# Kernel optimization log

Measured on AMD Instinct MI355X. Metric: run time of the kernel, lower is better.

Reference implementation:

```python
import jax, jax.numpy as jnp
import numpy as np

B, D, H, G = 32768, 768, 256, 8
GS = D // G          # group size = 96
MIN_G, MAX_G = 2, 6  # min/max active groups


def setup_inputs() -> dict:
    key = jax.random.key(0)
    ks = jax.random.split(key, 12)
    s = 0.02
    return {
        "query_embedding": jax.random.normal(ks[0], (B, D), jnp.float32),
        # router_net: Linear(D,H) -> LayerNorm(H) -> GELU -> Linear(H,H//2) -> GELU -> Linear(H//2,G)
        "w1": jax.random.normal(ks[1], (D, H), jnp.float32) * s,
        "b1": jnp.zeros((H,), jnp.float32),
        "ln_g": jnp.ones((H,), jnp.float32),
        "ln_b": jnp.zeros((H,), jnp.float32),
        "w2": jax.random.normal(ks[2], (H, H // 2), jnp.float32) * s,
        "b2": jnp.zeros((H // 2,), jnp.float32),
        "w3": jax.random.normal(ks[3], (H // 2, G), jnp.float32) * s,
        "b3": jnp.zeros((G,), jnp.float32),
        # dim_importance: Linear(D,H) -> GELU -> Linear(H,D) (bias init 2.0) -> Sigmoid
        "dw1": jax.random.normal(ks[4], (D, H), jnp.float32) * s,
        "db1": jnp.zeros((H,), jnp.float32),
        "dw2": jax.random.normal(ks[5], (H, D), jnp.float32) * s,
        "db2": jnp.full((D,), 2.0, jnp.float32),
        "group_importance": jax.random.normal(ks[6], (G,), jnp.float32) * s,
    }


def _gelu(x):
    return jax.nn.gelu(x, approximate=False)  # torch nn.GELU default = exact erf


def _layernorm(x, g, b, eps=1e-5):
    mu = jnp.mean(x, axis=-1, keepdims=True)
    var = jnp.var(x, axis=-1, keepdims=True)
    return (x - mu) * jax.lax.rsqrt(var + eps) * g + b


def reference(query_embedding, w1, b1, ln_g, ln_b, w2, b2, w3, b3,
              dw1, db1, dw2, db2, group_importance):
    x = query_embedding
    # router_net (eval mode: dropout is identity, sigmoid gating not gumbel)
    h1 = _gelu(_layernorm(x @ w1 + b1, ln_g, ln_b))
    h2 = _gelu(h1 @ w2 + b2)
    group_logits = h2 @ w3 + b3 + group_importance          # [B, G]
    group_probs = jax.nn.sigmoid(group_logits)

    # constrained hard selection: top MIN_G always on; ranks MIN_G..MAX_G-1 on iff prob > 0.5
    order = jnp.argsort(-group_probs, axis=-1)              # descending sort indices [B, G]
    sorted_probs = jnp.take_along_axis(group_probs, order, axis=-1)
    ranks = jnp.arange(G)
    act_sorted = jnp.where(ranks < MIN_G, 1.0,
                           jnp.where(ranks < MAX_G,
                                     (sorted_probs > 0.5).astype(jnp.float32), 0.0))
    b_idx = jnp.arange(x.shape[0])[:, None]
    hard_mask = jnp.zeros_like(group_probs).at[b_idx, order].set(act_sorted)
    # straight-through estimator
    group_selection = hard_mask - jax.lax.stop_gradient(group_probs) + group_probs

    # expand each group decision over its group_size dims -> [B, D]
    group_mask = jnp.repeat(group_selection, GS, axis=-1)

    dim_weights = jax.nn.sigmoid(_gelu(x @ dw1 + db1) @ dw2 + db2)  # [B, D]
    mask = group_mask * dim_weights

    active_groups = jnp.mean(jnp.sum((group_probs > 0.5).astype(jnp.float32), axis=-1))
    group_usage = jnp.mean((group_probs > 0.5).astype(jnp.float32), axis=0)
    f = jnp.mean(group_probs, axis=0)
    load_balance = G * jnp.sum(f * (1.0 / G))
    active_dims = jnp.mean(jnp.sum((mask > 0.5).astype(jnp.float32), axis=-1))

    return (mask, group_mask, dim_weights, group_probs, group_selection,
            active_groups, group_usage, load_balance, active_dims)
```

## Files before the change

### kernel.cpp

```cpp
#include <hip/hip_runtime.h>
#include <math.h>

#define NB 32768
#define ND 768
#define NH 256
#define NG 8
#define GSZ 96

typedef __attribute__((ext_vector_type(8))) short short8_t;
typedef __attribute__((ext_vector_type(4))) float f32x4;

__device__ __forceinline__ float gelu_exact(float v) {
    return 0.5f * v * (1.0f + erff(v * 0.7071067811865475f));
}
__device__ __forceinline__ float sigmoidf_(float v) {
    return 1.0f / (1.0f + expf(-v));
}
__device__ __forceinline__ unsigned short f2bf(float f) {
    union { float f; unsigned u; } a; a.f = f;
    unsigned r = a.u + 0x7FFF + ((a.u >> 16) & 1);
    return (unsigned short)(r >> 16);
}
__device__ __forceinline__ void f2bf2(float f, unsigned short& hi, unsigned short& lo) {
    union { float f; unsigned u; } a; a.f = f;
    unsigned r = a.u + 0x7FFF + ((a.u >> 16) & 1);
    hi = (unsigned short)(r >> 16);
    union { unsigned u; float f; } hf; hf.u = (r >> 16) << 16;
    float rem = f - hf.f;
    union { float f; unsigned u; } b; b.f = rem;
    unsigned r2 = b.u + 0x7FFF + ((b.u >> 16) & 1);
    lo = (unsigned short)(r2 >> 16);
}

__global__ __launch_bounds__(256) void cvt_wall(
    const float* __restrict__ w1, const float* __restrict__ dw1,
    const float* __restrict__ dw2, const float* __restrict__ w2,
    unsigned short* __restrict__ w1Th, unsigned short* __restrict__ w1Tl,
    unsigned short* __restrict__ dw1T, unsigned short* __restrict__ dw2T,
    unsigned short* __restrict__ w2Th, unsigned short* __restrict__ w2Tl,
    float* __restrict__ scal)
{
    const int b = blockIdx.x, t = threadIdx.x;
    if (b < 96) {
        int idx = b * 256 + t;
        int k8 = idx >> 8, c = idx & 255;
        short8_t h, lo;
        #pragma unroll
        for (int j = 0; j < 8; ++j) {
            unsigned short hi_, lo_;
            f2bf2(w1[(size_t)(k8 * 8 + j) * 256 + c], hi_, lo_);
            h[j] = (short)hi_; lo[j] = (short)lo_;
        }
        *(short8_t*)(w1Th + (size_t)c * 768 + k8 * 8) = h;
        *(short8_t*)(w1Tl + (size_t)c * 768 + k8 * 8) = lo;
    } else if (b < 192) {
        int idx = (b - 96) * 256 + t;
        int k8 = idx >> 8, c = idx & 255;
        short8_t h;
        #pragma unroll
        for (int j = 0; j < 8; ++j)
            h[j] = (short)f2bf(dw1[(size_t)(k8 * 8 + j) * 256 + c]);
        *(short8_t*)(dw1T + (size_t)c * 768 + k8 * 8) = h;
    } else if (b < 288) {
        int idx = (b - 192) * 256 + t;
        int k8 = idx / 768, c = idx - k8 * 768;
        short8_t h;
        #pragma unroll
        for (int j = 0; j < 8; ++j)
            h[j] = (short)f2bf(dw2[(size_t)(k8 * 8 + j) * 768 + c]);
        *(short8_t*)(dw2T + (size_t)c * 256 + k8 * 8) = h;
    } else if (b < 304) {
        int idx = (b - 288) * 256 + t;
        int k8 = idx >> 7, c = idx & 127;
        short8_t h, lo;
        #pragma unroll
        for (int j = 0; j < 8; ++j) {
            unsigned short hi_, lo_;
            f2bf2(w2[(size_t)(k8 * 8 + j) * 128 + c], hi_, lo_);
            h[j] = (short)hi_; lo[j] = (short)lo_;
        }
        *(short8_t*)(w2Th + (size_t)c * 256 + k8 * 8) = h;
        *(short8_t*)(w2Tl + (size_t)c * 256 + k8 * 8) = lo;
    } else {
        if (t < 11) scal[t] = 0.0f;
    }
}

__global__ __launch_bounds__(512) void mfma_pair(
    const float* __restrict__ x,
    const unsigned short* __restrict__ w1Th, const unsigned short* __restrict__ w1Tl,
    const unsigned short* __restrict__ dw1T, const float* __restrict__ db1,
    float* __restrict__ u1, unsigned short* __restrict__ g1h)
{
    __shared__ unsigned short Ah[128][40];
    __shared__ unsigned short Al[128][40];
    __shared__ unsigned short Bh[256][40];
    __shared__ unsigned short Bl[256][40];

    const int tid = threadIdx.x;
    const int l = tid & 63;
    const int w = tid >> 6;
    const int wm = w >> 2, wn = w & 3;
    const int lg = l >> 4, lr = l & 15;
    const bool splitRole = blockIdx.x < 256;
    const int rowsBase = (blockIdx.x & 255) * 128;

    f32x4 acc[4][4];
    #pragma unroll
    for (int mi = 0; mi < 4; ++mi)
        #pragma unroll
        for (int ni = 0; ni < 4; ++ni) acc[mi][ni] = (f32x4){0.f, 0.f, 0.f, 0.f};

    const int sArow = tid >> 2, sAseg = tid & 3;

    for (int kb = 0; kb < ND; kb += 32) {
        {
            const float* src = x + (size_t)(rowsBase + sArow) * ND + kb + sAseg * 8;
            float4 v0 = *(const float4*)src;
            float4 v1 = *(const float4*)(src + 4);
            float f[8] = {v0.x, v0.y, v0.z, v0.w, v1.x, v1.y, v1.z, v1.w};
            if (splitRole) {
                short8_t ph, pl;
                #pragma unroll
                for (int j = 0; j < 8; ++j) {
                    unsigned short hi_, lo_;
                    f2bf2(f[j], hi_, lo_);
                    ph[j] = (short)hi_; pl[j] = (short)lo_;
                }
                *(short8_t*)&Ah[sArow][sAseg * 8] = ph;
                *(short8_t*)&Al[sArow][sAseg * 8] = pl;
            } else {
                short8_t ph;
                #pragma unroll
                for (int j = 0; j < 8; ++j) ph[j] = (short)f2bf(f[j]);
                *(short8_t*)&Ah[sArow][sAseg * 8] = ph;
            }
        }
        #pragma unroll
        for (int m = 0; m < 2; ++m) {
            int flat = m * 512 + tid;
            int col = flat >> 2, seg = flat & 3;
            size_t off = (size_t)col * ND + kb + seg * 8;
            if (splitRole) {
                *(short8_t*)&Bh[col][seg * 8] = *(const short8_t*)(w1Th + off);
                *(short8_t*)&Bl[col][seg * 8] = *(const short8_t*)(w1Tl + off);
            } else {
                *(short8_t*)&Bh[col][seg * 8] = *(const short8_t*)(dw1T + off);
            }
        }
        __syncthreads();

        short8_t afh[4], bfh[4];
        #pragma unroll
        for (int mi = 0; mi < 4; ++mi)
            afh[mi] = *(const short8_t*)&Ah[wm * 64 + mi * 16 + lr][lg * 8];
        #pragma unroll
        for (int ni = 0; ni < 4; ++ni)
            bfh[ni] = *(const short8_t*)&Bh[wn * 64 + ni * 16 + lr][lg * 8];
        if (splitRole) {
            short8_t afl[4], bfl[4];
            #pragma unroll
            for (int mi = 0; mi < 4; ++mi)
                afl[mi] = *(const short8_t*)&Al[wm * 64 + mi * 16 + lr][lg * 8];
            #pragma unroll
            for (int ni = 0; ni < 4; ++ni)
                bfl[ni] = *(const short8_t*)&Bl[wn * 64 + ni * 16 + lr][lg * 8];
            #pragma unroll
            for (int mi = 0; mi < 4; ++mi)
                #pragma unroll
                for (int ni = 0; ni < 4; ++ni) {
                    acc[mi][ni] = __builtin_amdgcn_mfma_f32_16x16x32_bf16(
                        afl[mi], bfh[ni], acc[mi][ni], 0, 0, 0);
                    acc[mi][ni] = __builtin_amdgcn_mfma_f32_16x16x32_bf16(
                        afh[mi], bfl[ni], acc[mi][ni], 0, 0, 0);
                    acc[mi][ni] = __builtin_amdgcn_mfma_f32_16x16x32_bf16(
                        afh[mi], bfh[ni], acc[mi][ni], 0, 0, 0);
                }
        } else {
            #pragma unroll
            for (int mi = 0; mi < 4; ++mi)
                #pragma unroll
                for (int ni = 0; ni < 4; ++ni)
                    acc[mi][ni] = __builtin_amdgcn_mfma_f32_16x16x32_bf16(
                        afh[mi], bfh[ni], acc[mi][ni], 0, 0, 0);
        }
        __syncthreads();
    }

    if (splitRole) {
        #pragma unroll
        for (int ni = 0; ni < 4; ++ni) {
            int col = wn * 64 + ni * 16 + lr;
            #pragma unroll
            for (int mi = 0; mi < 4; ++mi) {
                int rbase = rowsBase + wm * 64 + mi * 16 + lg * 4;
                #pragma unroll
                for (int j = 0; j < 4; ++j)
                    u1[(size_t)(rbase + j) * 256 + col] = acc[mi][ni][j];
            }
        }
    } else {
        #pragma unroll
        for (int ni = 0; ni < 4; ++ni) {
            int col = wn * 64 + ni * 16 + lr;
            float bv = db1[col];
            #pragma unroll
            for (int mi = 0; mi < 4; ++mi) {
                int rbase = rowsBase + wm * 64 + mi * 16 + lg * 4;
                #pragma unroll
                for (int j = 0; j < 4; ++j)
                    g1h[(size_t)(rbase + j) * 256 + col] =
                        f2bf(gelu_exact(acc[mi][ni][j] + bv));
            }
        }
    }
}

__global__ __launch_bounds__(256) void k1_epi(
    const float* __restrict__ u1, const float* __restrict__ b1,
    const float* __restrict__ lng, const float* __restrict__ lnb,
    float* __restrict__ h1)
{
    const int wv = threadIdx.x >> 6, l = threadIdx.x & 63;
    const int row = blockIdx.x * 4 + wv;
    float4 a = *(const float4*)(u1 + (size_t)row * 256 + l * 4);
    float4 bb = *(const float4*)(b1 + l * 4);
    float u[4] = {a.x + bb.x, a.y + bb.y, a.z + bb.z, a.w + bb.w};
    float s = u[0] + u[1] + u[2] + u[3];
    float q = u[0]*u[0] + u[1]*u[1] + u[2]*u[2] + u[3]*u[3];
    #pragma unroll
    for (int o = 1; o < 64; o <<= 1) {
        s += __shfl_xor(s, o);
        q += __shfl_xor(q, o);
    }
    float mean = s * (1.0f / 256.0f);
    float var  = q * (1.0f / 256.0f) - mean * mean;
    float rstd = rsqrtf(var + 1e-5f);
    float4 g = *(const float4*)(lng + l * 4);
    float4 be = *(const float4*)(lnb + l * 4);
    float4 o;
    o.x = gelu_exact((u[0] - mean) * rstd * g.x + be.x);
    o.y = gelu_exact((u[1] - mean) * rstd * g.y + be.y);
    o.z = gelu_exact((u[2] - mean) * rstd * g.z + be.z);
    o.w = gelu_exact((u[3] - mean) * rstd * g.w + be.w);
    *(float4*)(h1 + (size_t)row * 256 + l * 4) = o;
}

__global__ __launch_bounds__(256) void mfma_u2(
    const float* __restrict__ h1, const unsigned short* __restrict__ BTh,
    const unsigned short* __restrict__ BTl, float* __restrict__ u2)
{
    __shared__ unsigned short Ah[128][40];
    __shared__ unsigned short Al[128][40];
    __shared__ unsigned short Bh[128][40];
    __shared__ unsigned short Bl[128][40];

    const int tid = threadIdx.x;
    const int l = tid & 63;
    const int w = tid >> 6;
    const int wm = w >> 1, wn = w & 1;
    const int lg = l >> 4, lr = l & 15;
    const int rowsBase = blockIdx.x * 128;

    f32x4 acc[4][4];
    #pragma unroll
    for (int mi = 0; mi < 4; ++mi)
        #pragma unroll
        for (int ni = 0; ni < 4; ++ni) acc[mi][ni] = (f32x4){0.f, 0.f, 0.f, 0.f};

    for (int kb = 0; kb < 256; kb += 32) {
        #pragma unroll
        for (int m = 0; m < 2; ++m) {
            int flat = m * 256 + tid;
            int row = flat >> 2, seg = flat & 3;
            const float* src = h1 + (size_t)(rowsBase + row) * 256 + kb + seg * 8;
            float4 v0 = *(const float4*)src;
            float4 v1 = *(const float4*)(src + 4);
            float f[8] = {v0.x, v0.y, v0.z, v0.w, v1.x, v1.y, v1.z, v1.w};
            short8_t ph, pl;
            #pragma unroll
            for (int j = 0; j < 8; ++j) {
                unsigned short hi_, lo_;
                f2bf2(f[j], hi_, lo_);
                ph[j] = (short)hi_; pl[j] = (short)lo_;
            }
            *(short8_t*)&Ah[row][seg * 8] = ph;
            *(short8_t*)&Al[row][seg * 8] = pl;
        }
        #pragma unroll
        for (int m = 0; m < 2; ++m) {
            int flat = m * 256 + tid;
            int col = flat >> 2, seg = flat & 3;
            size_t off = (size_t)col * 256 + kb + seg * 8;
            *(short8_t*)&Bh[col][seg * 8] = *(const short8_t*)(BTh + off);
            *(short8_t*)&Bl[col][seg * 8] = *(const short8_t*)(BTl + off);
        }
        __syncthreads();

        short8_t afh[4], afl[4], bfh[4], bfl[4];
        #pragma unroll
        for (int mi = 0; mi < 4; ++mi) {
            afh[mi] = *(const short8_t*)&Ah[wm * 64 + mi * 16 + lr][lg * 8];
            afl[mi] = *(const short8_t*)&Al[wm * 64 + mi * 16 + lr][lg * 8];
        }
        #pragma unroll
        for (int ni = 0; ni < 4; ++ni) {
            bfh[ni] = *(const short8_t*)&Bh[wn * 64 + ni * 16 + lr][lg * 8];
            bfl[ni] = *(const short8_t*)&Bl[wn * 64 + ni * 16 + lr][lg * 8];
        }
        #pragma unroll
        for (int mi = 0; mi < 4; ++mi)
            #pragma unroll
            for (int ni = 0; ni < 4; ++ni) {
                acc[mi][ni] = __builtin_amdgcn_mfma_f32_16x16x32_bf16(
                    afl[mi], bfh[ni], acc[mi][ni], 0, 0, 0);
                acc[mi][ni] = __builtin_amdgcn_mfma_f32_16x16x32_bf16(
                    afh[mi], bfl[ni], acc[mi][ni], 0, 0, 0);
                acc[mi][ni] = __builtin_amdgcn_mfma_f32_16x16x32_bf16(
                    afh[mi], bfh[ni], acc[mi][ni], 0, 0, 0);
            }
        __syncthreads();
    }

    #pragma unroll
    for (int ni = 0; ni < 4; ++ni) {
        int col = wn * 64 + ni * 16 + lr;
        #pragma unroll
        for (int mi = 0; mi < 4; ++mi) {
            int rbase = rowsBase + wm * 64 + mi * 16 + lg * 4;
            #pragma unroll
            for (int j = 0; j < 4; ++j)
                u2[(size_t)(rbase + j) * 128 + col] = acc[mi][ni][j];
        }
    }
}

__global__ __launch_bounds__(128) void k3_router(
    const float* __restrict__ u2, const float* __restrict__ w3,
    const float* __restrict__ b3, const float* __restrict__ gi,
    const float* __restrict__ b2, float* __restrict__ probsOut,
    float* __restrict__ selOut, float* __restrict__ scal)
{
    __shared__ float ws3[128][8];
    __shared__ float sAct[2], sP[2], sCnt[2][8];

    const int tid = threadIdx.x;
    *(float4*)&ws3[tid][0] = *(const float4*)(w3 + tid * 8);
    *(float4*)&ws3[tid][4] = *(const float4*)(w3 + tid * 8 + 4);
    __syncthreads();

    const int row = blockIdx.x * 128 + tid;
    const float* r0p = u2 + (size_t)row * 128;

    float accg[8];
    #pragma unroll
    for (int g = 0; g < 8; ++g) accg[g] = 0.0f;
    #pragma unroll 4
    for (int k4 = 0; k4 < 32; ++k4) {
        float4 a = *(const float4*)(r0p + k4 * 4);
        float4 bb = *(const float4*)(b2 + k4 * 4);
        float hv4[4];
        hv4[0] = gelu_exact(a.x + bb.x);
        hv4[1] = gelu_exact(a.y + bb.y);
        hv4[2] = gelu_exact(a.z + bb.z);
        hv4[3] = gelu_exact(a.w + bb.w);
        #pragma unroll
        for (int t = 0; t < 4; ++t)
            #pragma unroll
            for (int g = 0; g < 8; ++g)
                accg[g] = fmaf(hv4[t], ws3[k4 * 4 + t][g], accg[g]);
    }

    float p[8], gs[8], cnt[8];
    float actCnt = 0.0f, pSum = 0.0f;
    #pragma unroll
    for (int g = 0; g < 8; ++g) {
        float lg = accg[g] + b3[g] + gi[g];
        p[g] = sigmoidf_(lg);
    }
    #pragma unroll
    for (int g = 0; g < 8; ++g) {
        int rank = 0;
        #pragma unroll
        for (int j = 0; j < 8; ++j) {
            rank += (p[j] > p[g]) ? 1 : 0;
            rank += (j < g && p[j] == p[g]) ? 1 : 0;
        }
        float act = (rank < 2) ? 1.0f
                  : ((rank < 6) ? ((p[g] > 0.5f) ? 1.0f : 0.0f) : 0.0f);
        gs[g] = (act - p[g]) + p[g];
        float over = (p[g] > 0.5f) ? 1.0f : 0.0f;
        cnt[g] = over;
        actCnt += over;
        pSum += p[g];
    }

    *(float4*)(probsOut + (size_t)row * 8)     = *(float4*)&p[0];
    *(float4*)(probsOut + (size_t)row * 8 + 4) = *(float4*)&p[4];
    *(float4*)(selOut   + (size_t)row * 8)     = *(float4*)&gs[0];
    *(float4*)(selOut   + (size_t)row * 8 + 4) = *(float4*)&gs[4];

    #pragma unroll
    for (int o = 32; o > 0; o >>= 1) {
        actCnt += __shfl_down(actCnt, o);
        pSum   += __shfl_down(pSum, o);
        #pragma unroll
        for (int g = 0; g < 8; ++g) cnt[g] += __shfl_down(cnt[g], o);
    }
    if ((tid & 63) == 0) {
        int w = tid >> 6;
        sAct[w] = actCnt; sP[w] = pSum;
        #pragma unroll
        for (int g = 0; g < 8; ++g) sCnt[w][g] = cnt[g];
    }
    __syncthreads();
    if (tid == 0) {
        const float invB = 1.0f / 32768.0f;
        atomicAdd(&scal[0], (sAct[0] + sAct[1]) * invB);
        atomicAdd(&scal[9], (sP[0] + sP[1]) * invB);
        #pragma unroll
        for (int g = 0; g < 8; ++g)
            atomicAdd(&scal[1 + g], (sCnt[0][g] + sCnt[1][g]) * invB);
    }
}

__global__ __launch_bounds__(512) void mfma_dw2m(
    const unsigned short* __restrict__ g1h, const unsigned short* __restrict__ dw2T,
    const float* __restrict__ db2, const float* __restrict__ sel,
    float* __restrict__ dwts, float* __restrict__ maskOut,
    float* __restrict__ activeDims)
{
    __shared__ unsigned short As[128][40];
    __shared__ unsigned short Bs[256][40];
    __shared__ float sc[8];

    const int tid = threadIdx.x;
    const int l = tid & 63;
    const int w = tid >> 6;
    const int wm = w >> 2, wn = w & 3;
    const int lg = l >> 4, lr = l & 15;
    const int rb = blockIdx.x / 3, cb = blockIdx.x - rb * 3;
    const int rowsBase = rb * 128, colBase = cb * 256;

    f32x4 acc[4][4];
    #pragma unroll
    for (int mi = 0; mi < 4; ++mi)
        #pragma unroll
        for (int ni = 0; ni < 4; ++ni) acc[mi][ni] = (f32x4){0.f, 0.f, 0.f, 0.f};

    const int sArow = tid >> 2, sAseg = tid & 3;

    for (int kb = 0; kb < 256; kb += 32) {
        *(short8_t*)&As[sArow][sAseg * 8] =
            *(const short8_t*)(g1h + (size_t)(rowsBase + sArow) * 256 + kb + sAseg * 8);
        #pragma unroll
        for (int m = 0; m < 2; ++m) {
            int flat = m * 512 + tid;
            int col = flat >> 2, seg = flat & 3;
            *(short8_t*)&Bs[col][seg * 8] =
                *(const short8_t*)(dw2T + (size_t)(colBase + col) * 256 + kb + seg * 8);
        }
        __syncthreads();

        short8_t af[4], bf[4];
        #pragma unroll
        for (int mi = 0; mi < 4; ++mi)
            af[mi] = *(const short8_t*)&As[wm * 64 + mi * 16 + lr][lg * 8];
        #pragma unroll
        for (int ni = 0; ni < 4; ++ni)
            bf[ni] = *(const short8_t*)&Bs[wn * 64 + ni * 16 + lr][lg * 8];
        #pragma unroll
        for (int mi = 0; mi < 4; ++mi)
            #pragma unroll
            for (int ni = 0; ni < 4; ++ni)
                acc[mi][ni] = __builtin_amdgcn_mfma_f32_16x16x32_bf16(
                    af[mi], bf[ni], acc[mi][ni], 0, 0, 0);
        __syncthreads();
    }

    float cntF = 0.0f;
    #pragma unroll
    for (int ni = 0; ni < 4; ++ni) {
        int col = colBase + wn * 64 + ni * 16 + lr;
        float bv = db2[col];
        int g = col / GSZ;
        #pragma unroll
        for (int mi = 0; mi < 4; ++mi) {
            int rbase = rowsBase + wm * 64 + mi * 16 + lg * 4;
            #pragma unroll
            for (int j = 0; j < 4; ++j) {
                int row = rbase + j;
                float v = sigmoidf_(acc[mi][ni][j] + bv);
                dwts[(size_t)row * 768 + col] = v;
                float m = sel[(size_t)row * 8 + g] * v;
                maskOut[(size_t)row * 768 + col] = m;
                cntF += (m > 0.5f) ? 1.0f : 0.0f;
            }
        }
    }
    #pragma unroll
    for (int o = 32; o > 0; o >>= 1) cntF += __shfl_down(cntF, o);
    if ((tid & 63) == 0) sc[tid >> 6] = cntF;
    __syncthreads();
    if (tid == 0)
        atomicAdd(activeDims, (sc[0] + sc[1] + sc[2] + sc[3] +
                               sc[4] + sc[5] + sc[6] + sc[7]) * (1.0f / 32768.0f));
}

__global__ __launch_bounds__(256) void k4_gmask(
    const float* __restrict__ sel, float* __restrict__ gmaskOut)
{
    const int stride = gridDim.x * 256;
    for (int i4 = blockIdx.x * 256 + threadIdx.x; i4 < 6291456; i4 += stride) {
        int row = i4 / 192;
        int rem = i4 - row * 192;
        int g = rem / 24;
        float v = sel[(size_t)row * 8 + g];
        float4 gm = {v, v, v, v};
        *(float4*)(gmaskOut + (size_t)i4 * 4) = gm;
    }
}

extern "C" void kernel_launch(void* const* d_in, const int* in_sizes, int n_in,
                              void* d_out, int out_size, void* d_ws, size_t ws_size,
                              hipStream_t stream)
{
    const float* x   = (const float*)d_in[0];
    const float* w1  = (const float*)d_in[1];
    const float* b1  = (const float*)d_in[2];
    const float* lng = (const float*)d_in[3];
    const float* lnb = (const float*)d_in[4];
    const float* w2  = (const float*)d_in[5];
    const float* b2  = (const float*)d_in[6];
    const float* w3  = (const float*)d_in[7];
    const float* b3  = (const float*)d_in[8];
    const float* dw1 = (const float*)d_in[9];
    const float* db1 = (const float*)d_in[10];
    const float* dw2 = (const float*)d_in[11];
    const float* db2 = (const float*)d_in[12];
    const float* gi  = (const float*)d_in[13];

    float* out   = (float*)d_out;
    float* mask  = out;
    float* gmask = out + 25165824;
    float* dwts  = out + 50331648;
    float* probs = out + 75497472;
    float* sel   = out + 75759616;
    float* scal  = out + 76021760;

    float* u1 = mask;
    float* h1 = mask + 8388608;
    float* u2 = mask + 16777216;
    unsigned short* g1h  = (unsigned short*)gmask;
    unsigned short* w1Th = (unsigned short*)(gmask + 4194304);
    unsigned short* w1Tl = (unsigned short*)(gmask + 4292608);
    unsigned short* dw1T = (unsigned short*)(gmask + 4390912);
    unsigned short* dw2T = (unsigned short*)(gmask + 4489216);
    unsigned short* w2Th = (unsigned short*)(gmask + 4587520);
    unsigned short* w2Tl = (unsigned short*)(gmask + 4603904);

    cvt_wall<<<dim3(305), dim3(256), 0, stream>>>(
        w1, dw1, dw2, w2, w1Th, w1Tl, dw1T, dw2T, w2Th, w2Tl, scal);
    mfma_pair<<<dim3(512), dim3(512), 0, stream>>>(
        x, w1Th, w1Tl, dw1T, db1, u1, g1h);
    k1_epi<<<dim3(8192), dim3(256), 0, stream>>>(u1, b1, lng, lnb, h1);
    mfma_u2<<<dim3(256), dim3(256), 0, stream>>>(h1, w2Th, w2Tl, u2);
    k3_router<<<dim3(256), dim3(128), 0, stream>>>(
        u2, w3, b3, gi, b2, probs, sel, scal);
    mfma_dw2m<<<dim3(768), dim3(512), 0, stream>>>(
        g1h, dw2T, db2, sel, dwts, mask, &scal[10]);
    k4_gmask<<<dim3(2048), dim3(256), 0, stream>>>(sel, gmask);
}
```

Before: 290.1 us.

## Fuse router head into u2 GEMM and write group mask in dw2 epilogue

Merges the k3_router kernel into the h1@w2 MFMA kernel. The epilogue applies GELU, does the w3 projection with cross-lane shuffles and shared-memory partials, then runs the top-k selection, so u2 is never written to or read back from global memory. When a workspace buffer is provided, scratch bf16 tensors move there and the group mask is written directly in the dw2 epilogue, removing the separate k4_gmask pass. The cost is more shared memory, a heavier epilogue in the u2 GEMM, and a dependence on the workspace being supplied.

```diff
diff --git a/kernel.cpp b/kernel.cpp
--- a/kernel.cpp
+++ b/kernel.cpp
@@ -246,14 +246,20 @@
     *(float4*)(h1 + (size_t)row * 256 + l * 4) = o;
 }
 
-__global__ __launch_bounds__(256) void mfma_u2(
+__global__ __launch_bounds__(256) void mfma_u2r(
     const float* __restrict__ h1, const unsigned short* __restrict__ BTh,
-    const unsigned short* __restrict__ BTl, float* __restrict__ u2)
+    const unsigned short* __restrict__ BTl, const float* __restrict__ b2,
+    const float* __restrict__ w3, const float* __restrict__ b3,
+    const float* __restrict__ gi, float* __restrict__ probsOut,
+    float* __restrict__ selOut, float* __restrict__ scal)
 {
     __shared__ unsigned short Ah[128][40];
     __shared__ unsigned short Al[128][40];
     __shared__ unsigned short Bh[128][40];
     __shared__ unsigned short Bl[128][40];
+    __shared__ float ws3[128][8];
+    __shared__ float sLog[2][128][8];
+    __shared__ float sAct[2], sP[2], sCnt[2][8];
 
     const int tid = threadIdx.x;
     const int l = tid & 63;
@@ -261,6 +267,11 @@
     const int wm = w >> 1, wn = w & 1;
     const int lg = l >> 4, lr = l & 15;
     const int rowsBase = blockIdx.x * 128;
+
+    if (tid < 128) {
+        *(float4*)&ws3[tid][0] = *(const float4*)(w3 + tid * 8);
+        *(float4*)&ws3[tid][4] = *(const float4*)(w3 + tid * 8 + 4);
+    }
 
     f32x4 acc[4][4];
     #pragma unroll
@@ -322,83 +333,71 @@
         __syncthreads();
     }
 
-    #pragma unroll
-    for (int ni = 0; ni < 4; ++ni) {
-        int col = wn * 64 + ni * 16 + lr;
-        #pragma unroll
-        for (int mi = 0; mi < 4; ++mi) {
-            int rbase = rowsBase + wm * 64 + mi * 16 + lg * 4;
-            #pragma unroll
-            for (int j = 0; j < 4; ++j)
-                u2[(size_t)(rbase + j) * 128 + col] = acc[mi][ni][j];
-        }
-    }
-}
-
-__global__ __launch_bounds__(128) void k3_router(
-    const float* __restrict__ u2, const float* __restrict__ w3,
-    const float* __restrict__ b3, const float* __restrict__ gi,
-    const float* __restrict__ b2, float* __restrict__ probsOut,
-    float* __restrict__ selOut, float* __restrict__ scal)
-{
-    __shared__ float ws3[128][8];
-    __shared__ float sAct[2], sP[2], sCnt[2][8];
-
-    const int tid = threadIdx.x;
-    *(float4*)&ws3[tid][0] = *(const float4*)(w3 + tid * 8);
-    *(float4*)&ws3[tid][4] = *(const float4*)(w3 + tid * 8 + 4);
+    float b2c[4];
+    #pragma unroll
+    for (int ni = 0; ni < 4; ++ni) b2c[ni] = b2[wn * 64 + ni * 16 + lr];
+
+    #pragma unroll
+    for (int mi = 0; mi < 4; ++mi) {
+        #pragma unroll
+        for (int j = 0; j < 4; ++j) {
+            float pl[8];
+            #pragma unroll
+            for (int g = 0; g < 8; ++g) pl[g] = 0.f;
+            #pragma unroll
+            for (int ni = 0; ni < 4; ++ni) {
+                int c = wn * 64 + ni * 16 + lr;
+                float h2v = gelu_exact(acc[mi][ni][j] + b2c[ni]);
+                #pragma unroll
+                for (int g = 0; g < 8; ++g)
+                    pl[g] = fmaf(h2v, ws3[c][g], pl[g]);
+            }
+            #pragma unroll
+            for (int o = 1; o < 16; o <<= 1)
+                #pragma unroll
+                for (int g = 0; g < 8; ++g) pl[g] += __shfl_xor(pl[g], o);
+            if (lr == 0) {
+                int rl = wm * 64 + mi * 16 + lg * 4 + j;
+                #pragma unroll
+                for (int g = 0; g < 8; ++g) sLog[wn][rl][g] = pl[g];
+            }
+        }
+    }
     __syncthreads();
-
-    const int row = blockIdx.x * 128 + tid;
-    const float* r0p = u2 + (size_t)row * 128;
-
-    float accg[8];
-    #pragma unroll
-    for (int g = 0; g < 8; ++g) accg[g] = 0.0f;
-    #pragma unroll 4
-    for (int k4 = 0; k4 < 32; ++k4) {
-        float4 a = *(const float4*)(r0p + k4 * 4);
-        float4 bb = *(const float4*)(b2 + k4 * 4);
-        float hv4[4];
-        hv4[0] = gelu_exact(a.x + bb.x);
-        hv4[1] = gelu_exact(a.y + bb.y);
-        hv4[2] = gelu_exact(a.z + bb.z);
-        hv4[3] = gelu_exact(a.w + bb.w);
-        #pragma unroll
-        for (int t = 0; t < 4; ++t)
-            #pragma unroll
-            for (int g = 0; g < 8; ++g)
-                accg[g] = fmaf(hv4[t], ws3[k4 * 4 + t][g], accg[g]);
-    }
 
     float p[8], gs[8], cnt[8];
     float actCnt = 0.0f, pSum = 0.0f;
     #pragma unroll
-    for (int g = 0; g < 8; ++g) {
-        float lg = accg[g] + b3[g] + gi[g];
-        p[g] = sigmoidf_(lg);
-    }
-    #pragma unroll
-    for (int g = 0; g < 8; ++g) {
-        int rank = 0;
-        #pragma unroll
-        for (int j = 0; j < 8; ++j) {
-            rank += (p[j] > p[g]) ? 1 : 0;
-            rank += (j < g && p[j] == p[g]) ? 1 : 0;
-        }
-        float act = (rank < 2) ? 1.0f
-                  : ((rank < 6) ? ((p[g] > 0.5f) ? 1.0f : 0.0f) : 0.0f);
-        gs[g] = (act - p[g]) + p[g];
-        float over = (p[g] > 0.5f) ? 1.0f : 0.0f;
-        cnt[g] = over;
-        actCnt += over;
-        pSum += p[g];
-    }
-
-    *(float4*)(probsOut + (size_t)row * 8)     = *(float4*)&p[0];
-    *(float4*)(probsOut + (size_t)row * 8 + 4) = *(float4*)&p[4];
-    *(float4*)(selOut   + (size_t)row * 8)     = *(float4*)&gs[0];
-    *(float4*)(selOut   + (size_t)row * 8 + 4) = *(float4*)&gs[4];
+    for (int g = 0; g < 8; ++g) cnt[g] = 0.0f;
+
+    if (tid < 128) {
+        int row = rowsBase + tid;
+        #pragma unroll
+        for (int g = 0; g < 8; ++g) {
+            float lg_ = sLog[0][tid][g] + sLog[1][tid][g] + b3[g] + gi[g];
+            p[g] = sigmoidf_(lg_);
+        }
+        #pragma unroll
+        for (int g = 0; g < 8; ++g) {
+            int rank = 0;
+            #pragma unroll
+            for (int j = 0; j < 8; ++j) {
+                rank += (p[j] > p[g]) ? 1 : 0;
+                rank += (j < g && p[j] == p[g]) ? 1 : 0;
+            }
+            float act = (rank < 2) ? 1.0f
+                      : ((rank < 6) ? ((p[g] > 0.5f) ? 1.0f : 0.0f) : 0.0f);
+            gs[g] = (act - p[g]) + p[g];
+            float over = (p[g] > 0.5f) ? 1.0f : 0.0f;
+            cnt[g] = over;
+            actCnt += over;
+            pSum += p[g];
+        }
+        *(float4*)(probsOut + (size_t)row * 8)     = *(float4*)&p[0];
+        *(float4*)(probsOut + (size_t)row * 8 + 4) = *(float4*)&p[4];
+        *(float4*)(selOut   + (size_t)row * 8)     = *(float4*)&gs[0];
+        *(float4*)(selOut   + (size_t)row * 8 + 4) = *(float4*)&gs[4];
+    }
 
     #pragma unroll
     for (int o = 32; o > 0; o >>= 1) {
@@ -407,11 +406,11 @@
         #pragma unroll
         for (int g = 0; g < 8; ++g) cnt[g] += __shfl_down(cnt[g], o);
     }
-    if ((tid & 63) == 0) {
-        int w = tid >> 6;
-        sAct[w] = actCnt; sP[w] = pSum;
-        #pragma unroll
-        for (int g = 0; g < 8; ++g) sCnt[w][g] = cnt[g];
+    if (tid < 128 && (tid & 63) == 0) {
+        int wv_ = tid >> 6;
+        sAct[wv_] = actCnt; sP[wv_] = pSum;
+        #pragma unroll
+        for (int g = 0; g < 8; ++g) sCnt[wv_][g] = cnt[g];
     }
     __syncthreads();
     if (tid == 0) {
@@ -428,7 +427,7 @@
     const unsigned short* __restrict__ g1h, const unsigned short* __restrict__ dw2T,
     const float* __restrict__ db2, const float* __restrict__ sel,
     float* __restrict__ dwts, float* __restrict__ maskOut,
-    float* __restrict__ activeDims)
+    float* __restrict__ gmaskOut, float* __restrict__ activeDims)
 {
     __shared__ unsigned short As[128][40];
     __shared__ unsigned short Bs[256][40];
@@ -490,10 +489,12 @@
             #pragma unroll
             for (int j = 0; j < 4; ++j) {
                 int row = rbase + j;
+                float sv = sel[(size_t)row * 8 + g];
                 float v = sigmoidf_(acc[mi][ni][j] + bv);
                 dwts[(size_t)row * 768 + col] = v;
-                float m = sel[(size_t)row * 8 + g] * v;
+                float m = sv * v;
                 maskOut[(size_t)row * 768 + col] = m;
+                if (gmaskOut) gmaskOut[(size_t)row * 768 + col] = sv;
                 cntF += (m > 0.5f) ? 1.0f : 0.0f;
             }
         }
@@ -550,24 +551,41 @@
 
     float* u1 = mask;
     float* h1 = mask + 8388608;
-    float* u2 = mask + 16777216;
-    unsigned short* g1h  = (unsigned short*)gmask;
-    unsigned short* w1Th = (unsigned short*)(gmask + 4194304);
-    unsigned short* w1Tl = (unsigned short*)(gmask + 4292608);
-    unsigned short* dw1T = (unsigned short*)(gmask + 4390912);
-    unsigned short* dw2T = (unsigned short*)(gmask + 4489216);
-    unsigned short* w2Th = (unsigned short*)(gmask + 4587520);
-    unsigned short* w2Tl = (unsigned short*)(gmask + 4603904);
+
+    const size_t WS_NEED = 16777216ULL
+                         + 393216ULL * 4
+                         + 65536ULL * 2;
+    bool useWs = (d_ws != nullptr) && (ws_size >= WS_NEED);
+
+    unsigned short *g1h, *w1Th, *w1Tl, *dw1T, *dw2T, *w2Th, *w2Tl;
+    if (useWs) {
+        char* wsb = (char*)d_ws;
+        g1h  = (unsigned short*)(wsb);
+        w1Th = (unsigned short*)(wsb + 16777216);
+        w1Tl = (unsigned short*)(wsb + 16777216 + 393216);
+        dw1T = (unsigned short*)(wsb + 16777216 + 393216 * 2);
+        dw2T = (unsigned short*)(wsb + 16777216 + 393216 * 3);
+        w2Th = (unsigned short*)(wsb + 16777216 + 393216 * 4);
+        w2Tl = (unsigned short*)(wsb + 16777216 + 393216 * 4 + 65536);
+    } else {
+        g1h  = (unsigned short*)gmask;
+        w1Th = (unsigned short*)(gmask + 4194304);
+        w1Tl = (unsigned short*)(gmask + 4292608);
+        dw1T = (unsigned short*)(gmask + 4390912);
+        dw2T = (unsigned short*)(gmask + 4489216);
+        w2Th = (unsigned short*)(gmask + 4587520);
+        w2Tl = (unsigned short*)(gmask + 4603904);
+    }
 
     cvt_wall<<<dim3(305), dim3(256), 0, stream>>>(
         w1, dw1, dw2, w2, w1Th, w1Tl, dw1T, dw2T, w2Th, w2Tl, scal);
     mfma_pair<<<dim3(512), dim3(512), 0, stream>>>(
         x, w1Th, w1Tl, dw1T, db1, u1, g1h);
     k1_epi<<<dim3(8192), dim3(256), 0, stream>>>(u1, b1, lng, lnb, h1);
-    mfma_u2<<<dim3(256), dim3(256), 0, stream>>>(h1, w2Th, w2Tl, u2);
-    k3_router<<<dim3(256), dim3(128), 0, stream>>>(
-        u2, w3, b3, gi, b2, probs, sel, scal);
+    mfma_u2r<<<dim3(256), dim3(256), 0, stream>>>(
+        h1, w2Th, w2Tl, b2, w3, b3, gi, probs, sel, scal);
     mfma_dw2m<<<dim3(768), dim3(512), 0, stream>>>(
-        g1h, dw2T, db2, sel, dwts, mask, &scal[10]);
-    k4_gmask<<<dim3(2048), dim3(256), 0, stream>>>(sel, gmask);
-}
+        g1h, dw2T, db2, sel, dwts, mask, useWs ? gmask : nullptr, &scal[10]);
+    if (!useWs)
+        k4_gmask<<<dim3(2048), dim3(256), 0, stream>>>(sel, gmask);
+}
```

Result: slower. 304.9 us (+5.1%).
